# Kernel optimization log

Hardware: AMD Instinct MI355X
Metric: run time of the kernel (lower is better)

Reference implementation:

```python
import jax, jax.numpy as jnp
import numpy as np

B, S, D, DI = 8, 4096, 512, 2048
EPS = 1e-12  # torch F.normalize eps


def _l2norm(x):
    n = jnp.sqrt(jnp.sum(x * x, axis=-1, keepdims=True))
    return x / jnp.maximum(n, EPS)


def setup_inputs() -> dict:
    key = jax.random.key(0)
    ks = jax.random.split(key, 10)
    sd = 1.0 / np.sqrt(D)
    si = 1.0 / np.sqrt(DI)
    return {
        "x": jax.random.normal(ks[0], (B, S, D), jnp.float32),
        "wq": jax.random.uniform(ks[1], (D, DI), jnp.float32, -sd, sd),
        "wk": jax.random.uniform(ks[2], (D, DI), jnp.float32, -sd, sd),
        "wv": jax.random.uniform(ks[3], (D, DI), jnp.float32, -sd, sd),
        "wo": jax.random.uniform(ks[4], (DI, D), jnp.float32, -si, si),
        "w1": jax.random.uniform(ks[5], (D, DI), jnp.float32, -sd, sd),
        "b1": jax.random.uniform(ks[6], (DI,), jnp.float32, -sd, sd),
        "w2": jax.random.uniform(ks[7], (DI, D), jnp.float32, -si, si),
        "b2": jax.random.uniform(ks[8], (D,), jnp.float32, -si, si),
    }


def reference(x, wq, wk, wv, wo, w1, b1, w2, b2):
    # Hydra attention (linear): normalize(q) * sum_s(normalize(k)*v)
    q = _l2norm(jnp.einsum('bsd,de->bse', x, wq))
    k = _l2norm(jnp.einsum('bsd,de->bse', x, wk))
    v = jnp.einsum('bsd,de->bse', x, wv)
    kv = jnp.sum(k * v, axis=-2, keepdims=True)  # [B,1,DI]
    attn = jnp.einsum('bse,ed->bsd', q * kv, wo) + x  # dropout = identity (eval)
    # position-wise FFN with residual
    h = jax.nn.relu(jnp.einsum('bsd,de->bse', attn, w1) + b1)
    out = jnp.einsum('bse,ed->bsd', h, w2) + b2 + attn
    return out
```

## Files before the change

### kernel.cpp

```cpp
#include <hip/hip_runtime.h>
#include <stdint.h>

#define Bb  8
#define Ss  4096
#define Dd  512
#define DIi 2048
#define Mm  (Bb*Ss)

typedef unsigned short u16;
typedef __bf16 bf16x8 __attribute__((ext_vector_type(8)));
typedef float  f32x4  __attribute__((ext_vector_type(4)));

__device__ __forceinline__ float bfu(unsigned int u) {
  return __uint_as_float((u & 0xffffu) << 16);
}
__device__ __forceinline__ u16 f2bu(float f) {
  unsigned int x = __float_as_uint(f);
  return (u16)((x + 0x7fffu + ((x >> 16) & 1u)) >> 16);
}

__device__ __forceinline__ void tr_tile(const float* __restrict__ W, u16* __restrict__ Wt,
                                        int K, int N, int local, int tid) {
  __shared__ float t[32][33];
  const int nx = N / 32;
  const int n0 = (local % nx) * 32, k0 = (local / nx) * 32;
  const int tx = tid & 31, ty = tid >> 5;
#pragma unroll
  for (int i = 0; i < 32; i += 8)
    t[ty + i][tx] = W[(long)(k0 + ty + i) * N + n0 + tx];
  __syncthreads();
#pragma unroll
  for (int i = 0; i < 32; i += 8)
    Wt[(long)(n0 + ty + i) * K + k0 + tx] = f2bu(t[tx][ty + i]);
}

__global__ __launch_bounds__(256) void prep(
    const float* __restrict__ x, u16* __restrict__ xb,
    const float* wk, const float* wv, const float* w1,
    const float* wo, const float* w2, const float* wq,
    u16* wkT, u16* wvT, u16* w1T, u16* woT, u16* w2T, u16* wqb,
    float* __restrict__ zptr) {
  const int bid = blockIdx.x, tid = threadIdx.x;
  if (bid < 320) {
    zptr[bid * 256 + tid] = 0.f;
  } else if (bid < 2368) {
    long i = (long)(bid - 320) * 256 + tid;
    const long n4 = (long)Mm * Dd / 4;
    const long st = 2048L * 256;
    for (; i < n4; i += st) {
      float4 v = ((const float4*)x)[i];
      ushort4 o;
      o.x = f2bu(v.x); o.y = f2bu(v.y); o.z = f2bu(v.z); o.w = f2bu(v.w);
      ((ushort4*)xb)[i] = o;
    }
  } else if (bid < 3392)  tr_tile(wk, wkT, Dd, DIi, bid - 2368, tid);
  else if (bid < 4416)    tr_tile(wv, wvT, Dd, DIi, bid - 3392, tid);
  else if (bid < 5440)    tr_tile(w1, w1T, Dd, DIi, bid - 4416, tid);
  else if (bid < 6464)    tr_tile(wo, woT, DIi, Dd, bid - 5440, tid);
  else if (bid < 7488)    tr_tile(w2, w2T, DIi, Dd, bid - 6464, tid);
  else {
    long i = (long)(bid - 7488) * 256 + tid;
    float4 v = ((const float4*)wq)[i];
    ushort4 o;
    o.x = f2bu(v.x); o.y = f2bu(v.y); o.z = f2bu(v.z); o.w = f2bu(v.w);
    ((ushort4*)wqb)[i] = o;
  }
}

__global__ __launch_bounds__(256) void build_wob(const u16* __restrict__ woT,
                                                 const float* __restrict__ kv,
                                                 u16* __restrict__ wob) {
  const int b = blockIdx.y;
  long i = (long)blockIdx.x * 256 + threadIdx.x;
  const long tot = (long)Dd * DIi / 8;
  if (i >= tot) return;
  const long e = i * 8;
  const int k = (int)(e & (DIi - 1));
  ushort4 w0 = *(const ushort4*)(woT + e);
  ushort4 w1 = *(const ushort4*)(woT + e + 4);
  const float* kvp = kv + (long)b * DIi + k;
  ushort4 o0, o1;
  o0.x = f2bu(bfu(w0.x) * kvp[0]); o0.y = f2bu(bfu(w0.y) * kvp[1]);
  o0.z = f2bu(bfu(w0.z) * kvp[2]); o0.w = f2bu(bfu(w0.w) * kvp[3]);
  o1.x = f2bu(bfu(w1.x) * kvp[4]); o1.y = f2bu(bfu(w1.y) * kvp[5]);
  o1.z = f2bu(bfu(w1.z) * kvp[6]); o1.w = f2bu(bfu(w1.w) * kvp[7]);
  u16* dst = wob + (long)b * Dd * DIi + e;
  *(ushort4*)dst = o0;
  *(ushort4*)(dst + 4) = o1;
}

#define GLL(src, dst) \
  __builtin_amdgcn_global_load_lds((const __attribute__((address_space(1))) unsigned int*)(src), \
                                   (__attribute__((address_space(3))) unsigned int*)(dst), 16, 0, 0)

enum { G_PROJ = 0, G_FFN1 = 2, G_FFN2 = 3, G_KV = 4 };

template<int MODE>
__global__ __launch_bounds__(512, 2) void gemm8(
    const u16* __restrict__ A, const u16* __restrict__ Bt,
    int N, int K,
    u16* __restrict__ Ybf, float* __restrict__ Yf,
    const u16* __restrict__ resb, const float* __restrict__ bias,
    float* __restrict__ nsq, const float* __restrict__ nsqIn,
    const u16* __restrict__ Kst, float* __restrict__ kvout)
{
  __shared__ u16 lds8[65536];

  const int bx = blockIdx.x;
  const int by = blockIdx.y;
  const int tid  = threadIdx.x;
  const int lane = tid & 63;
  const int wid  = tid >> 6;
  const int wr = wid >> 2, wc = wid & 3;
  const int l15 = lane & 15, lg = lane >> 4;

  const long bm0 = (long)by * 256;
  const long bn0 = (long)bx * 256;
  const int NT = K >> 6;

  const int bq = (int)(bm0 >> 12);
  const u16* pA = A + bm0 * K;
  const u16* pB = Bt + bn0 * K;

  const int rowT = ((tid >> 6) << 3) | (tid & 7);
  const int cc8  = ((tid >> 3) & 7) * 8;

#define STAGE(PTR, LD, H, TT, BUFU, REGU) do {                                  \
    const u16* s0_ = (PTR) + (size_t)((H) * 128 + rowT) * (LD)                  \
                     + (size_t)(TT) * 64 + cc8;                                 \
    u16* d_ = lds8 + (BUFU) + (REGU) + (H) * 8192 + wid * 512;                  \
    GLL(s0_, d_);                                                               \
    GLL(s0_ + (size_t)64 * (LD), d_ + 4096);                                    \
  } while (0)

  const int aoff = (wr * 16384 + (l15 >> 3) * 1024 + lg * 128 + (l15 & 7) * 16) >> 1;
  const int boff = (32768 + (wc >> 1) * 16384 + (wc & 1) * 8192 +
                    (l15 >> 3) * 1024 + lg * 128 + (l15 & 7) * 16) >> 1;
#define LDA(M_, KS_, BU_) (*(const bf16x8*)(lds8 + (BU_) + aoff + (M_) * 1024 + (KS_) * 256))
#define LDB(N_, KS_, BU_) (*(const bf16x8*)(lds8 + (BU_) + boff + (N_) * 1024 + (KS_) * 256))

  f32x4 acc[8][4] = {};

  STAGE(pA, K, 0, 0, 0, 0);
  STAGE(pA, K, 1, 0, 0, 0);
  STAGE(pB, K, 0, 0, 0, 16384);
  STAGE(pB, K, 1, 0, 0, 16384);
  STAGE(pA, K, 0, 1, 32768, 0);
  asm volatile("s_waitcnt vmcnt(2)" ::: "memory");
  __builtin_amdgcn_s_barrier();

  for (int t = 0; t < NT; ++t) {
    const int bufu = (t & 1) * 32768;
    const int nbuf = bufu ^ 32768;
    bf16x8 aF[4], bF[4];

#pragma unroll
    for (int n = 0; n < 4; ++n) bF[n] = LDB(n, 0, bufu);
#pragma unroll
    for (int m = 0; m < 4; ++m) aF[m] = LDA(m, 0, bufu);
    if (t + 1 < NT) STAGE(pA, K, 1, t + 1, nbuf, 0);
    __builtin_amdgcn_s_barrier();
    __builtin_amdgcn_s_setprio(1);
#pragma unroll
    for (int m = 0; m < 4; ++m)
#pragma unroll
      for (int n = 0; n < 4; ++n)
        acc[m][n] = __builtin_amdgcn_mfma_f32_16x16x32_bf16(aF[m], bF[n], acc[m][n], 0, 0, 0);
    __builtin_amdgcn_s_setprio(0);

#pragma unroll
    for (int m = 0; m < 4; ++m) aF[m] = LDA(4 + m, 0, bufu);
    if (t + 1 < NT) STAGE(pB, K, 0, t + 1, nbuf, 16384);
    __builtin_amdgcn_s_barrier();
    __builtin_amdgcn_s_setprio(1);
#pragma unroll
    for (int m = 0; m < 4; ++m)
#pragma unroll
      for (int n = 0; n < 4; ++n)
        acc[4 + m][n] = __builtin_amdgcn_mfma_f32_16x16x32_bf16(aF[m], bF[n], acc[4 + m][n], 0, 0, 0);
    __builtin_amdgcn_s_setprio(0);

#pragma unroll
    for (int n = 0; n < 4; ++n) bF[n] = LDB(n, 1, bufu);
#pragma unroll
    for (int m = 0; m < 4; ++m) aF[m] = LDA(m, 1, bufu);
    if (t + 1 < NT) STAGE(pB, K, 1, t + 1, nbuf, 16384);
    __builtin_amdgcn_s_barrier();
    __builtin_amdgcn_s_setprio(1);
#pragma unroll
    for (int m = 0; m < 4; ++m)
#pragma unroll
      for (int n = 0; n < 4; ++n)
        acc[m][n] = __builtin_amdgcn_mfma_f32_16x16x32_bf16(aF[m], bF[n], acc[m][n], 0, 0, 0);
    __builtin_amdgcn_s_setprio(0);

#pragma unroll
    for (int m = 0; m < 4; ++m) aF[m] = LDA(4 + m, 1, bufu);
    __builtin_amdgcn_s_barrier();
    __builtin_amdgcn_s_setprio(1);
#pragma unroll
    for (int m = 0; m < 4; ++m)
#pragma unroll
      for (int n = 0; n < 4; ++n)
        acc[4 + m][n] = __builtin_amdgcn_mfma_f32_16x16x32_bf16(aF[m], bF[n], acc[4 + m][n], 0, 0, 0);
    __builtin_amdgcn_s_setprio(0);

    if (t + 1 < NT) {
      __builtin_amdgcn_s_barrier();
      if (t + 2 < NT) {
        STAGE(pA, K, 0, t + 2, bufu, 0);
        asm volatile("s_waitcnt vmcnt(2)" ::: "memory");
      } else {
        asm volatile("s_waitcnt vmcnt(0)" ::: "memory");
      }
      __builtin_amdgcn_s_barrier();
    }
  }

  if constexpr (MODE == G_KV) {
    __syncthreads();
#pragma unroll
    for (int i = 0; i < 16; ++i) {
      const int r_ = i * 16 + wid * 2 + (lane >> 5);
      const int c_ = (lane & 31) ^ (r_ & 15);
      const u16* src = Kst + (size_t)(bm0 + r_) * N + bn0 + c_ * 8;
      u16* d_ = lds8 + i * 4096 + wid * 512;
      GLL(src, d_);
    }
    asm volatile("s_waitcnt vmcnt(0)" ::: "memory");
    __builtin_amdgcn_s_barrier();

    const int col4 = wc * 64 + l15;
    float cs[4] = {0.f, 0.f, 0.f, 0.f};
#pragma unroll
    for (int m = 0; m < 8; ++m) {
      const long row0g = bm0 + wr * 128 + m * 16 + lg * 4;
      float rn4[4];
#pragma unroll
      for (int r = 0; r < 4; ++r)
        rn4[r] = 1.f / fmaxf(sqrtf(nsqIn[row0g + r]), 1e-12f);
#pragma unroll
      for (int n = 0; n < 4; ++n) {
        const int col = col4 + n * 16;
#pragma unroll
        for (int r = 0; r < 4; ++r) {
          const int krow = wr * 128 + m * 16 + lg * 4 + r;
          const int byte_ = krow * 512 + (((col >> 3) ^ (krow & 15)) << 4) + (col & 7) * 2;
          const float kvl = bfu(*(const u16*)((const char*)lds8 + byte_));
          cs[n] += kvl * rn4[r] * acc[m][n][r];
        }
      }
    }
#pragma unroll
    for (int n = 0; n < 4; ++n) {
      cs[n] += __shfl_xor(cs[n], 16, 64);
      cs[n] += __shfl_xor(cs[n], 32, 64);
    }
    if (lane < 16) {
#pragma unroll
      for (int n = 0; n < 4; ++n) {
        const long col = bn0 + wc * 64 + n * 16 + l15;
        atomicAdd(&kvout[(long)bq * DIi + col], cs[n]);
      }
    }
  } else if constexpr (MODE == G_PROJ) {
    float sk[32];
#pragma unroll
    for (int i = 0; i < 32; ++i) sk[i] = 0.f;
#pragma unroll
    for (int m = 0; m < 8; ++m) {
      const long row0 = bm0 + wr * 128 + m * 16 + lg * 4;
#pragma unroll
      for (int n = 0; n < 4; ++n) {
        const long col = bn0 + wc * 64 + n * 16 + l15;
#pragma unroll
        for (int r = 0; r < 4; ++r) {
          const float v = acc[m][n][r];
          Ybf[(row0 + r) * N + col] = f2bu(v);
          sk[m * 4 + r] += v * v;
        }
      }
    }
#pragma unroll
    for (int i = 0; i < 32; ++i) {
#pragma unroll
      for (int off = 1; off < 16; off <<= 1)
        sk[i] += __shfl_xor(sk[i], off, 64);
    }
    if (l15 == 0) {
#pragma unroll
      for (int m = 0; m < 8; ++m)
#pragma unroll
        for (int r = 0; r < 4; ++r)
          atomicAdd(&nsq[bm0 + wr * 128 + m * 16 + lg * 4 + r], sk[m * 4 + r]);
    }
  } else {
#pragma unroll
    for (int m = 0; m < 8; ++m) {
      const long row0 = bm0 + wr * 128 + m * 16 + lg * 4;
#pragma unroll
      for (int n = 0; n < 4; ++n) {
        const long col = bn0 + wc * 64 + n * 16 + l15;
#pragma unroll
        for (int r = 0; r < 4; ++r) {
          const long idx = (row0 + r) * N + col;
          const float v = acc[m][n][r];
          if constexpr (MODE == G_FFN1) {
            float o = v + bias[col];
            o = o > 0.f ? o : 0.f;
            Ybf[idx] = f2bu(o);
          } else {
            Yf[idx] = v + bias[col] + bfu(resb[idx]);
          }
        }
      }
    }
  }
#undef STAGE
#undef LDA
#undef LDB
}

__global__ __launch_bounds__(256) void mega_small(
    const u16* __restrict__ wqb, const u16* __restrict__ wob,
    u16* __restrict__ Gt, u16* __restrict__ Ut)
{
  __shared__ u16 As[4096];
  __shared__ u16 Bs[4096];
  const int K = DIi;
  const int z = blockIdx.z;
  const u16* Bt = (z == 0) ? wqb : wob + (size_t)(z - 1) * Dd * DIi;
  u16* Ct = (z == 0) ? Gt : Ut + (size_t)(z - 1) * Dd * Dd;

  const int tid = threadIdx.x, lane = tid & 63, w = tid >> 6;
  const int wr = w >> 1, wc = w & 1;
  const int l15 = lane & 15, lg = lane >> 4;
  const long bm0 = (long)blockIdx.y * 128;
  const long bn0 = (long)blockIdx.x * 128;

  const int c0 = tid, c1 = tid + 256;
  const u16* aS0 = wqb + (bm0 + (c0 >> 2)) * K + (c0 & 3) * 8;
  const u16* aS1 = wqb + (bm0 + (c1 >> 2)) * K + (c1 & 3) * 8;
  const u16* bS0 = Bt  + (bn0 + (c0 >> 2)) * K + (c0 & 3) * 8;
  const u16* bS1 = Bt  + (bn0 + (c1 >> 2)) * K + (c1 & 3) * 8;
  u16* aD0 = As + w * 512;
  u16* aD1 = As + 2048 + w * 512;
  u16* bD0 = Bs + w * 512;
  u16* bD1 = Bs + 2048 + w * 512;

  f32x4 acc[4][4] = {};

  for (int k0 = 0; k0 < K; k0 += 32) {
    GLL(aS0 + k0, aD0);
    GLL(aS1 + k0, aD1);
    GLL(bS0 + k0, bD0);
    GLL(bS1 + k0, bD1);
    __syncthreads();
    bf16x8 af[4], bfv[4];
#pragma unroll
    for (int m = 0; m < 4; ++m)
      af[m] = *(const bf16x8*)(As + (wr * 64 + m * 16 + l15) * 32 + lg * 8);
#pragma unroll
    for (int n = 0; n < 4; ++n)
      bfv[n] = *(const bf16x8*)(Bs + (wc * 64 + n * 16 + l15) * 32 + lg * 8);
#pragma unroll
    for (int m = 0; m < 4; ++m)
#pragma unroll
      for (int n = 0; n < 4; ++n)
        acc[m][n] = __builtin_amdgcn_mfma_f32_16x16x32_bf16(af[m], bfv[n], acc[m][n], 0, 0, 0);
    __syncthreads();
  }

#pragma unroll
  for (int m = 0; m < 4; ++m) {
    const int row0 = (int)bm0 + wr * 64 + m * 16 + lg * 4;
#pragma unroll
    for (int n = 0; n < 4; ++n) {
      const int col = (int)bn0 + wc * 64 + n * 16 + l15;
      ushort4 o;
      o.x = f2bu(acc[m][n][0]); o.y = f2bu(acc[m][n][1]);
      o.z = f2bu(acc[m][n][2]); o.w = f2bu(acc[m][n][3]);
      *(ushort4*)(Ct + (size_t)col * Dd + row0) = o;
    }
  }
}

template<int MODE>
__global__ __launch_bounds__(256) void mega_nx(
    const u16* __restrict__ xb, const u16* __restrict__ Gt, const u16* __restrict__ Ut,
    float* __restrict__ nqsq, u16* __restrict__ attnb)
{
  __shared__ u16 As[4096];
  __shared__ u16 Bs[4096];
  __shared__ u16 xs[16384];
  const int K = Dd, N = Dd;

  const int tid = threadIdx.x, lane = tid & 63, w = tid >> 6;
  const int wr = w >> 1, wc = w & 1;
  const int l15 = lane & 15, lg = lane >> 4;
  const long bm0 = (long)blockIdx.y * 128;
  const long bn0 = (long)blockIdx.x * 128;
  const int bq = (int)(bm0 >> 12);
  const u16* Bt = (MODE == 0) ? Gt : Ut + (size_t)bq * Dd * Dd;

  const int c0 = tid, c1 = tid + 256;
  const u16* aS0 = xb + (bm0 + (c0 >> 2)) * K + (c0 & 3) * 8;
  const u16* aS1 = xb + (bm0 + (c1 >> 2)) * K + (c1 & 3) * 8;
  const u16* bS0 = Bt + (bn0 + (c0 >> 2)) * K + (c0 & 3) * 8;
  const u16* bS1 = Bt + (bn0 + (c1 >> 2)) * K + (c1 & 3) * 8;
  u16* aD0 = As + w * 512;
  u16* aD1 = As + 2048 + w * 512;
  u16* bD0 = Bs + w * 512;
  u16* bD1 = Bs + 2048 + w * 512;

  f32x4 acc[4][4] = {};

  for (int k0 = 0; k0 < K; k0 += 32) {
    GLL(aS0 + k0, aD0);
    GLL(aS1 + k0, aD1);
    GLL(bS0 + k0, bD0);
    GLL(bS1 + k0, bD1);
    __syncthreads();
    bf16x8 af[4], bfv[4];
#pragma unroll
    for (int m = 0; m < 4; ++m)
      af[m] = *(const bf16x8*)(As + (wr * 64 + m * 16 + l15) * 32 + lg * 8);
#pragma unroll
    for (int n = 0; n < 4; ++n)
      bfv[n] = *(const bf16x8*)(Bs + (wc * 64 + n * 16 + l15) * 32 + lg * 8);
#pragma unroll
    for (int m = 0; m < 4; ++m)
#pragma unroll
      for (int n = 0; n < 4; ++n)
        acc[m][n] = __builtin_amdgcn_mfma_f32_16x16x32_bf16(af[m], bfv[n], acc[m][n], 0, 0, 0);
    __syncthreads();
  }

#pragma unroll
  for (int i = 0; i < 8; ++i) {
    const int c = i * 256 + tid;
    const int rowL = c >> 4;
    const int srcslot = (c & 15) ^ (rowL & 15);
    const u16* src = xb + (size_t)(bm0 + rowL) * Dd + bn0 + srcslot * 8;
    GLL(src, xs + i * 2048 + w * 512);
  }
  asm volatile("s_waitcnt vmcnt(0)" ::: "memory");
  __builtin_amdgcn_s_barrier();

#define XV(RL, CL) bfu(xs[(RL) * 128 + ((((CL) >> 3) ^ ((RL) & 15)) << 3) + ((CL) & 7)])

  if constexpr (MODE == 0) {
    float sk[16];
#pragma unroll
    for (int i = 0; i < 16; ++i) sk[i] = 0.f;
#pragma unroll
    for (int m = 0; m < 4; ++m) {
#pragma unroll
      for (int n = 0; n < 4; ++n) {
        const int colL = wc * 64 + n * 16 + l15;
#pragma unroll
        for (int r = 0; r < 4; ++r) {
          const int rowL = wr * 64 + m * 16 + lg * 4 + r;
          sk[m * 4 + r] += acc[m][n][r] * XV(rowL, colL);
        }
      }
    }
#pragma unroll
    for (int i = 0; i < 16; ++i) {
#pragma unroll
      for (int off = 1; off < 16; off <<= 1)
        sk[i] += __shfl_xor(sk[i], off, 64);
    }
    if (l15 == 0) {
#pragma unroll
      for (int m = 0; m < 4; ++m)
#pragma unroll
        for (int r = 0; r < 4; ++r)
          atomicAdd(&nqsq[bm0 + wr * 64 + m * 16 + lg * 4 + r], sk[m * 4 + r]);
    }
  } else {
#pragma unroll
    for (int m = 0; m < 4; ++m) {
      const long row0 = bm0 + wr * 64 + m * 16 + lg * 4;
      float rq[4];
#pragma unroll
      for (int r = 0; r < 4; ++r)
        rq[r] = 1.f / fmaxf(sqrtf(fmaxf(nqsq[row0 + r], 0.f)), 1e-12f);
#pragma unroll
      for (int n = 0; n < 4; ++n) {
        const int colL = wc * 64 + n * 16 + l15;
#pragma unroll
        for (int r = 0; r < 4; ++r) {
          const int rowL = wr * 64 + m * 16 + lg * 4 + r;
          attnb[(row0 + r) * N + bn0 + colL] = f2bu(acc[m][n][r] * rq[r] + XV(rowL, colL));
        }
      }
    }
  }
#undef XV
}

extern "C" void kernel_launch(void* const* d_in, const int* in_sizes, int n_in,
                              void* d_out, int out_size, void* d_ws, size_t ws_size,
                              hipStream_t stream) {
  const float* x  = (const float*)d_in[0];
  const float* wq = (const float*)d_in[1];
  const float* wk = (const float*)d_in[2];
  const float* wv = (const float*)d_in[3];
  const float* wo = (const float*)d_in[4];
  const float* w1 = (const float*)d_in[5];
  const float* b1 = (const float*)d_in[6];
  const float* w2 = (const float*)d_in[7];
  const float* b2 = (const float*)d_in[8];
  float* out = (float*)d_out;

  char* p = (char*)d_ws;
  auto take = [&](size_t bytes) {
    char* r = p; p += (bytes + 255) & ~(size_t)255; return r;
  };
  u16*   xb    = (u16*)take((size_t)Mm * Dd * 2);
  u16*   wkT   = (u16*)take((size_t)DIi * Dd * 2);
  u16*   wvT   = (u16*)take((size_t)DIi * Dd * 2);
  u16*   woT   = (u16*)take((size_t)Dd * DIi * 2);
  u16*   w1T   = (u16*)take((size_t)DIi * Dd * 2);
  u16*   w2T   = (u16*)take((size_t)Dd * DIi * 2);
  u16*   wqb   = (u16*)take((size_t)Dd * DIi * 2);
  u16*   wob   = (u16*)take((size_t)Bb * Dd * DIi * 2);
  u16*   Gt    = (u16*)take((size_t)Dd * Dd * 2);
  u16*   Ut    = (u16*)take((size_t)Bb * Dd * Dd * 2);
  u16*   buf1  = (u16*)take((size_t)Mm * DIi * 2);
  u16*   attnb = (u16*)take((size_t)Mm * Dd * 2);
  float* nksq  = (float*)take((size_t)Mm * 4);
  float* nqsq  = (float*)take((size_t)Mm * 4);
  float* kvp   = (float*)take((size_t)Bb * DIi * 4);
  (void)in_sizes; (void)n_in; (void)out_size; (void)ws_size;

  prep<<<8512, 256, 0, stream>>>(x, xb, wk, wv, w1, wo, w2, wq,
                                 wkT, wvT, w1T, woT, w2T, wqb, nksq);

  gemm8<G_PROJ><<<dim3(DIi / 256, Mm / 256), 512, 0, stream>>>(
      xb, wkT, DIi, Dd, buf1, nullptr, nullptr, nullptr, nksq, nullptr,
      nullptr, nullptr);

  gemm8<G_KV><<<dim3(DIi / 256, Mm / 256), 512, 0, stream>>>(
      xb, wvT, DIi, Dd, nullptr, nullptr, nullptr, nullptr, nullptr, nksq,
      buf1, kvp);

  build_wob<<<dim3((Dd * DIi / 8 + 255) / 256, Bb), 256, 0, stream>>>(woT, kvp, wob);

  mega_small<<<dim3(4, 4, 9), 256, 0, stream>>>(wqb, wob, Gt, Ut);

  mega_nx<0><<<dim3(4, Mm / 128), 256, 0, stream>>>(xb, Gt, nullptr, nqsq, nullptr);

  mega_nx<1><<<dim3(4, Mm / 128), 256, 0, stream>>>(xb, nullptr, Ut, nqsq, attnb);

  gemm8<G_FFN1><<<dim3(DIi / 256, Mm / 256), 512, 0, stream>>>(
      attnb, w1T, DIi, Dd, buf1, nullptr, nullptr, b1, nullptr, nullptr,
      nullptr, nullptr);

  gemm8<G_FFN2><<<dim3(Dd / 256, Mm / 256), 512, 0, stream>>>(
      buf1, w2T, Dd, DIi, nullptr, out, attnb, b2, nullptr, nullptr,
      nullptr, nullptr);
}
```

Before: 547.5 us.

## Compute key norms and kv via Gram matrices instead of full K/V projections

Removes the two full-size x·Wk and x·Wv GEMMs over all tokens. Key row norms now come from x·(Wk·Wkᵀ)·xᵀ through the existing Gram-style norm kernel. kv is computed as the column sums of Wk ∘ (Wvᵀ-side product of (x/|k|)ᵀ·x) per batch, using a transposed x, two small batched GEMMs and a column-sum kernel. This trades the large M×DI×D work for D×D×S per-batch GEMMs plus extra transposes and launches. Reassociating the sums in bf16 changes rounding.

```diff
diff --git a/kernel.cpp b/kernel.cpp
--- a/kernel.cpp
+++ b/kernel.cpp
@@ -36,15 +36,15 @@
 
 __global__ __launch_bounds__(256) void prep(
     const float* __restrict__ x, u16* __restrict__ xb,
-    const float* wk, const float* wv, const float* w1,
-    const float* wo, const float* w2, const float* wq,
-    u16* wkT, u16* wvT, u16* w1T, u16* woT, u16* w2T, u16* wqb,
+    const float* wv, const float* w1, const float* wo, const float* w2,
+    const float* wq, const float* wk,
+    u16* wvT, u16* w1T, u16* woT, u16* w2T, u16* wqb, u16* wkb,
     float* __restrict__ zptr) {
   const int bid = blockIdx.x, tid = threadIdx.x;
-  if (bid < 320) {
+  if (bid < 256) {
     zptr[bid * 256 + tid] = 0.f;
-  } else if (bid < 2368) {
-    long i = (long)(bid - 320) * 256 + tid;
+  } else if (bid < 2304) {
+    long i = (long)(bid - 256) * 256 + tid;
     const long n4 = (long)Mm * Dd / 4;
     const long st = 2048L * 256;
     for (; i < n4; i += st) {
@@ -53,17 +53,22 @@
       o.x = f2bu(v.x); o.y = f2bu(v.y); o.z = f2bu(v.z); o.w = f2bu(v.w);
       ((ushort4*)xb)[i] = o;
     }
-  } else if (bid < 3392)  tr_tile(wk, wkT, Dd, DIi, bid - 2368, tid);
-  else if (bid < 4416)    tr_tile(wv, wvT, Dd, DIi, bid - 3392, tid);
-  else if (bid < 5440)    tr_tile(w1, w1T, Dd, DIi, bid - 4416, tid);
-  else if (bid < 6464)    tr_tile(wo, woT, DIi, Dd, bid - 5440, tid);
-  else if (bid < 7488)    tr_tile(w2, w2T, DIi, Dd, bid - 6464, tid);
-  else {
-    long i = (long)(bid - 7488) * 256 + tid;
+  } else if (bid < 3328)  tr_tile(wv, wvT, Dd, DIi, bid - 2304, tid);
+  else if (bid < 4352)    tr_tile(w1, w1T, Dd, DIi, bid - 3328, tid);
+  else if (bid < 5376)    tr_tile(wo, woT, DIi, Dd, bid - 4352, tid);
+  else if (bid < 6400)    tr_tile(w2, w2T, DIi, Dd, bid - 5376, tid);
+  else if (bid < 7424) {
+    long i = (long)(bid - 6400) * 256 + tid;
     float4 v = ((const float4*)wq)[i];
     ushort4 o;
     o.x = f2bu(v.x); o.y = f2bu(v.y); o.z = f2bu(v.z); o.w = f2bu(v.w);
     ((ushort4*)wqb)[i] = o;
+  } else {
+    long i = (long)(bid - 7424) * 256 + tid;
+    float4 v = ((const float4*)wk)[i];
+    ushort4 o;
+    o.x = f2bu(v.x); o.y = f2bu(v.y); o.z = f2bu(v.z); o.w = f2bu(v.w);
+    ((ushort4*)wkb)[i] = o;
   }
 }
 
@@ -89,20 +94,65 @@
   *(ushort4*)(dst + 4) = o1;
 }
 
+__global__ void tr_x(const u16* __restrict__ xb, const float* __restrict__ nksq,
+                     u16* __restrict__ xT, u16* __restrict__ xrnT) {
+  __shared__ u16 t[32][33];
+  __shared__ float rns[32];
+  const int b = blockIdx.z;
+  const int s0 = blockIdx.y * 32, d0 = blockIdx.x * 32;
+  const int tx = threadIdx.x, ty = threadIdx.y;
+  const size_t sbase = (size_t)b * Ss + s0;
+#pragma unroll
+  for (int i = 0; i < 32; i += 8)
+    t[ty + i][tx] = xb[(sbase + ty + i) * Dd + d0 + tx];
+  if (ty == 0) {
+    const float nk = fmaxf(nksq[sbase + tx], 0.f);
+    rns[tx] = 1.f / fmaxf(sqrtf(nk), 1e-12f);
+  }
+  __syncthreads();
+  const size_t dbase = (size_t)b * Dd + d0;
+#pragma unroll
+  for (int i = 0; i < 32; i += 8) {
+    const u16 v = t[tx][ty + i];
+    const size_t idx = (dbase + ty + i) * Ss + s0 + tx;
+    xT[idx] = v;
+    xrnT[idx] = f2bu(bfu(v) * rns[tx]);
+  }
+}
+
+__global__ __launch_bounds__(256) void colsum_kv(const u16* __restrict__ wkb,
+                                                 const u16* __restrict__ Tb,
+                                                 float* __restrict__ kv) {
+  const int b = blockIdx.y;
+  const int e0 = blockIdx.x * 1024 + threadIdx.x * 4;
+  const u16* wp = wkb + e0;
+  const u16* tp = Tb + (size_t)b * Dd * DIi + e0;
+  float a0 = 0, a1 = 0, a2 = 0, a3 = 0;
+  for (int d = 0; d < Dd; ++d) {
+    ushort4 w = *(const ushort4*)wp;
+    ushort4 t = *(const ushort4*)tp;
+    a0 += bfu(w.x) * bfu(t.x);
+    a1 += bfu(w.y) * bfu(t.y);
+    a2 += bfu(w.z) * bfu(t.z);
+    a3 += bfu(w.w) * bfu(t.w);
+    wp += DIi; tp += DIi;
+  }
+  float* o = kv + (size_t)b * DIi + e0;
+  o[0] = a0; o[1] = a1; o[2] = a2; o[3] = a3;
+}
+
 #define GLL(src, dst) \
   __builtin_amdgcn_global_load_lds((const __attribute__((address_space(1))) unsigned int*)(src), \
                                    (__attribute__((address_space(3))) unsigned int*)(dst), 16, 0, 0)
 
-enum { G_PROJ = 0, G_FFN1 = 2, G_FFN2 = 3, G_KV = 4 };
+enum { G_FFN1 = 2, G_FFN2 = 3 };
 
 template<int MODE>
 __global__ __launch_bounds__(512, 2) void gemm8(
     const u16* __restrict__ A, const u16* __restrict__ Bt,
     int N, int K,
     u16* __restrict__ Ybf, float* __restrict__ Yf,
-    const u16* __restrict__ resb, const float* __restrict__ bias,
-    float* __restrict__ nsq, const float* __restrict__ nsqIn,
-    const u16* __restrict__ Kst, float* __restrict__ kvout)
+    const u16* __restrict__ resb, const float* __restrict__ bias)
 {
   __shared__ u16 lds8[65536];
 
@@ -118,7 +168,6 @@
   const long bn0 = (long)bx * 256;
   const int NT = K >> 6;
 
-  const int bq = (int)(bm0 >> 12);
   const u16* pA = A + bm0 * K;
   const u16* pB = Bt + bn0 * K;
 
@@ -217,101 +266,22 @@
     }
   }
 
-  if constexpr (MODE == G_KV) {
-    __syncthreads();
-#pragma unroll
-    for (int i = 0; i < 16; ++i) {
-      const int r_ = i * 16 + wid * 2 + (lane >> 5);
-      const int c_ = (lane & 31) ^ (r_ & 15);
-      const u16* src = Kst + (size_t)(bm0 + r_) * N + bn0 + c_ * 8;
-      u16* d_ = lds8 + i * 4096 + wid * 512;
-      GLL(src, d_);
-    }
-    asm volatile("s_waitcnt vmcnt(0)" ::: "memory");
-    __builtin_amdgcn_s_barrier();
-
-    const int col4 = wc * 64 + l15;
-    float cs[4] = {0.f, 0.f, 0.f, 0.f};
-#pragma unroll
-    for (int m = 0; m < 8; ++m) {
-      const long row0g = bm0 + wr * 128 + m * 16 + lg * 4;
-      float rn4[4];
-#pragma unroll
-      for (int r = 0; r < 4; ++r)
-        rn4[r] = 1.f / fmaxf(sqrtf(nsqIn[row0g + r]), 1e-12f);
-#pragma unroll
-      for (int n = 0; n < 4; ++n) {
-        const int col = col4 + n * 16;
-#pragma unroll
-        for (int r = 0; r < 4; ++r) {
-          const int krow = wr * 128 + m * 16 + lg * 4 + r;
-          const int byte_ = krow * 512 + (((col >> 3) ^ (krow & 15)) << 4) + (col & 7) * 2;
-          const float kvl = bfu(*(const u16*)((const char*)lds8 + byte_));
-          cs[n] += kvl * rn4[r] * acc[m][n][r];
-        }
-      }
-    }
+#pragma unroll
+  for (int m = 0; m < 8; ++m) {
+    const long row0 = bm0 + wr * 128 + m * 16 + lg * 4;
 #pragma unroll
     for (int n = 0; n < 4; ++n) {
-      cs[n] += __shfl_xor(cs[n], 16, 64);
-      cs[n] += __shfl_xor(cs[n], 32, 64);
-    }
-    if (lane < 16) {
-#pragma unroll
-      for (int n = 0; n < 4; ++n) {
-        const long col = bn0 + wc * 64 + n * 16 + l15;
-        atomicAdd(&kvout[(long)bq * DIi + col], cs[n]);
-      }
-    }
-  } else if constexpr (MODE == G_PROJ) {
-    float sk[32];
-#pragma unroll
-    for (int i = 0; i < 32; ++i) sk[i] = 0.f;
-#pragma unroll
-    for (int m = 0; m < 8; ++m) {
-      const long row0 = bm0 + wr * 128 + m * 16 + lg * 4;
-#pragma unroll
-      for (int n = 0; n < 4; ++n) {
-        const long col = bn0 + wc * 64 + n * 16 + l15;
-#pragma unroll
-        for (int r = 0; r < 4; ++r) {
-          const float v = acc[m][n][r];
-          Ybf[(row0 + r) * N + col] = f2bu(v);
-          sk[m * 4 + r] += v * v;
-        }
-      }
-    }
-#pragma unroll
-    for (int i = 0; i < 32; ++i) {
-#pragma unroll
-      for (int off = 1; off < 16; off <<= 1)
-        sk[i] += __shfl_xor(sk[i], off, 64);
-    }
-    if (l15 == 0) {
-#pragma unroll
-      for (int m = 0; m < 8; ++m)
-#pragma unroll
-        for (int r = 0; r < 4; ++r)
-          atomicAdd(&nsq[bm0 + wr * 128 + m * 16 + lg * 4 + r], sk[m * 4 + r]);
-    }
-  } else {
-#pragma unroll
-    for (int m = 0; m < 8; ++m) {
-      const long row0 = bm0 + wr * 128 + m * 16 + lg * 4;
-#pragma unroll
-      for (int n = 0; n < 4; ++n) {
-        const long col = bn0 + wc * 64 + n * 16 + l15;
-#pragma unroll
-        for (int r = 0; r < 4; ++r) {
-          const long idx = (row0 + r) * N + col;
-          const float v = acc[m][n][r];
-          if constexpr (MODE == G_FFN1) {
-            float o = v + bias[col];
-            o = o > 0.f ? o : 0.f;
-            Ybf[idx] = f2bu(o);
-          } else {
-            Yf[idx] = v + bias[col] + bfu(resb[idx]);
-          }
+      const long col = bn0 + wc * 64 + n * 16 + l15;
+#pragma unroll
+      for (int r = 0; r < 4; ++r) {
+        const long idx = (row0 + r) * N + col;
+        const float v = acc[m][n][r];
+        if constexpr (MODE == G_FFN1) {
+          float o = v + bias[col];
+          o = o > 0.f ? o : 0.f;
+          Ybf[idx] = f2bu(o);
+        } else {
+          Yf[idx] = v + bias[col] + bfu(resb[idx]);
         }
       }
     }
@@ -322,15 +292,19 @@
 }
 
 __global__ __launch_bounds__(256) void mega_small(
-    const u16* __restrict__ wqb, const u16* __restrict__ wob,
-    u16* __restrict__ Gt, u16* __restrict__ Ut)
+    const u16* __restrict__ wqb, const u16* __restrict__ wkb,
+    const u16* __restrict__ wob,
+    u16* __restrict__ Gt, u16* __restrict__ Gkt, u16* __restrict__ Ut, int zbase)
 {
   __shared__ u16 As[4096];
   __shared__ u16 Bs[4096];
   const int K = DIi;
-  const int z = blockIdx.z;
-  const u16* Bt = (z == 0) ? wqb : wob + (size_t)(z - 1) * Dd * DIi;
-  u16* Ct = (z == 0) ? Gt : Ut + (size_t)(z - 1) * Dd * Dd;
+  const int idx = blockIdx.z + zbase;
+  const u16* A  = (idx == 1) ? wkb : wqb;
+  const u16* Bt = (idx == 0) ? wqb : (idx == 1) ? wkb
+                  : wob + (size_t)(idx - 2) * Dd * DIi;
+  u16* Ct = (idx == 0) ? Gt : (idx == 1) ? Gkt
+            : Ut + (size_t)(idx - 2) * Dd * Dd;
 
   const int tid = threadIdx.x, lane = tid & 63, w = tid >> 6;
   const int wr = w >> 1, wc = w & 1;
@@ -339,10 +313,10 @@
   const long bn0 = (long)blockIdx.x * 128;
 
   const int c0 = tid, c1 = tid + 256;
-  const u16* aS0 = wqb + (bm0 + (c0 >> 2)) * K + (c0 & 3) * 8;
-  const u16* aS1 = wqb + (bm0 + (c1 >> 2)) * K + (c1 & 3) * 8;
-  const u16* bS0 = Bt  + (bn0 + (c0 >> 2)) * K + (c0 & 3) * 8;
-  const u16* bS1 = Bt  + (bn0 + (c1 >> 2)) * K + (c1 & 3) * 8;
+  const u16* aS0 = A  + (bm0 + (c0 >> 2)) * K + (c0 & 3) * 8;
+  const u16* aS1 = A  + (bm0 + (c1 >> 2)) * K + (c1 & 3) * 8;
+  const u16* bS0 = Bt + (bn0 + (c0 >> 2)) * K + (c0 & 3) * 8;
+  const u16* bS1 = Bt + (bn0 + (c1 >> 2)) * K + (c1 & 3) * 8;
   u16* aD0 = As + w * 512;
   u16* aD1 = As + 2048 + w * 512;
   u16* bD0 = Bs + w * 512;
@@ -386,9 +360,74 @@
 }
 
 template<int MODE>
+__global__ __launch_bounds__(256) void mega128b(
+    const u16* __restrict__ A0, const u16* __restrict__ Bt0,
+    u16* __restrict__ C0, int N, int K)
+{
+  __shared__ u16 As[4096];
+  __shared__ u16 Bs[4096];
+  const int z = blockIdx.z;
+  const u16* A  = A0 + (size_t)z * (MODE == 0 ? (size_t)Dd * Ss : (size_t)Dd * Dd);
+  const u16* Bt = (MODE == 0) ? Bt0 + (size_t)z * Dd * Ss : Bt0;
+  u16* C = C0 + (size_t)z * (MODE == 0 ? (size_t)Dd * Dd : (size_t)Dd * DIi);
+
+  const int tid = threadIdx.x, lane = tid & 63, w = tid >> 6;
+  const int wr = w >> 1, wc = w & 1;
+  const int l15 = lane & 15, lg = lane >> 4;
+  const long bm0 = (long)blockIdx.y * 128;
+  const long bn0 = (long)blockIdx.x * 128;
+
+  const int c0 = tid, c1 = tid + 256;
+  const u16* aS0 = A  + (bm0 + (c0 >> 2)) * K + (c0 & 3) * 8;
+  const u16* aS1 = A  + (bm0 + (c1 >> 2)) * K + (c1 & 3) * 8;
+  const u16* bS0 = Bt + (bn0 + (c0 >> 2)) * K + (c0 & 3) * 8;
+  const u16* bS1 = Bt + (bn0 + (c1 >> 2)) * K + (c1 & 3) * 8;
+  u16* aD0 = As + w * 512;
+  u16* aD1 = As + 2048 + w * 512;
+  u16* bD0 = Bs + w * 512;
+  u16* bD1 = Bs + 2048 + w * 512;
+
+  f32x4 acc[4][4] = {};
+
+  for (int k0 = 0; k0 < K; k0 += 32) {
+    GLL(aS0 + k0, aD0);
+    GLL(aS1 + k0, aD1);
+    GLL(bS0 + k0, bD0);
+    GLL(bS1 + k0, bD1);
+    __syncthreads();
+    bf16x8 af[4], bfv[4];
+#pragma unroll
+    for (int m = 0; m < 4; ++m)
+      af[m] = *(const bf16x8*)(As + (wr * 64 + m * 16 + l15) * 32 + lg * 8);
+#pragma unroll
+    for (int n = 0; n < 4; ++n)
+      bfv[n] = *(const bf16x8*)(Bs + (wc * 64 + n * 16 + l15) * 32 + lg * 8);
+#pragma unroll
+    for (int m = 0; m < 4; ++m)
+#pragma unroll
+      for (int n = 0; n < 4; ++n)
+        acc[m][n] = __builtin_amdgcn_mfma_f32_16x16x32_bf16(af[m], bfv[n], acc[m][n], 0, 0, 0);
+    __syncthreads();
+  }
+
+#pragma unroll
+  for (int m = 0; m < 4; ++m) {
+    const long row0 = bm0 + wr * 64 + m * 16 + lg * 4;
+#pragma unroll
+    for (int n = 0; n < 4; ++n) {
+      const long col = bn0 + wc * 64 + n * 16 + l15;
+#pragma unroll
+      for (int r = 0; r < 4; ++r)
+        C[(row0 + r) * N + col] = f2bu(acc[m][n][r]);
+    }
+  }
+}
+
+template<int MODE>
 __global__ __launch_bounds__(256) void mega_nx(
-    const u16* __restrict__ xb, const u16* __restrict__ Gt, const u16* __restrict__ Ut,
-    float* __restrict__ nqsq, u16* __restrict__ attnb)
+    const u16* __restrict__ xb, const u16* __restrict__ Gt, const u16* __restrict__ Gkt,
+    const u16* __restrict__ Ut,
+    float* __restrict__ nqsq, float* __restrict__ nksq, u16* __restrict__ attnb)
 {
   __shared__ u16 As[4096];
   __shared__ u16 Bs[4096];
@@ -398,10 +437,12 @@
   const int tid = threadIdx.x, lane = tid & 63, w = tid >> 6;
   const int wr = w >> 1, wc = w & 1;
   const int l15 = lane & 15, lg = lane >> 4;
-  const long bm0 = (long)blockIdx.y * 128;
+  const bool isK = (MODE == 0) && (blockIdx.y >= Mm / 128);
+  const long bm0 = (long)(isK ? blockIdx.y - Mm / 128 : blockIdx.y) * 128;
   const long bn0 = (long)blockIdx.x * 128;
   const int bq = (int)(bm0 >> 12);
-  const u16* Bt = (MODE == 0) ? Gt : Ut + (size_t)bq * Dd * Dd;
+  const u16* Bt = (MODE == 0) ? (isK ? Gkt : Gt) : Ut + (size_t)bq * Dd * Dd;
+  float* nsq = (MODE == 0) ? (isK ? nksq : nqsq) : nqsq;
 
   const int c0 = tid, c1 = tid + 256;
   const u16* aS0 = xb + (bm0 + (c0 >> 2)) * K + (c0 & 3) * 8;
@@ -476,7 +517,7 @@
       for (int m = 0; m < 4; ++m)
 #pragma unroll
         for (int r = 0; r < 4; ++r)
-          atomicAdd(&nqsq[bm0 + wr * 64 + m * 16 + lg * 4 + r], sk[m * 4 + r]);
+          atomicAdd(&nsq[bm0 + wr * 64 + m * 16 + lg * 4 + r], sk[m * 4 + r]);
     }
   } else {
 #pragma unroll
@@ -519,46 +560,54 @@
     char* r = p; p += (bytes + 255) & ~(size_t)255; return r;
   };
   u16*   xb    = (u16*)take((size_t)Mm * Dd * 2);
-  u16*   wkT   = (u16*)take((size_t)DIi * Dd * 2);
   u16*   wvT   = (u16*)take((size_t)DIi * Dd * 2);
+  u16*   w1T   = (u16*)take((size_t)DIi * Dd * 2);
   u16*   woT   = (u16*)take((size_t)Dd * DIi * 2);
-  u16*   w1T   = (u16*)take((size_t)DIi * Dd * 2);
   u16*   w2T   = (u16*)take((size_t)Dd * DIi * 2);
   u16*   wqb   = (u16*)take((size_t)Dd * DIi * 2);
-  u16*   wob   = (u16*)take((size_t)Bb * Dd * DIi * 2);
+  u16*   wkb   = (u16*)take((size_t)Dd * DIi * 2);
   u16*   Gt    = (u16*)take((size_t)Dd * Dd * 2);
+  u16*   Gkt   = (u16*)take((size_t)Dd * Dd * 2);
   u16*   Ut    = (u16*)take((size_t)Bb * Dd * Dd * 2);
   u16*   buf1  = (u16*)take((size_t)Mm * DIi * 2);
   u16*   attnb = (u16*)take((size_t)Mm * Dd * 2);
   float* nksq  = (float*)take((size_t)Mm * 4);
   float* nqsq  = (float*)take((size_t)Mm * 4);
   float* kvp   = (float*)take((size_t)Bb * DIi * 4);
+  u16* xT   = buf1;
+  u16* xrnT = buf1 + (size_t)Mm * Dd;
+  u16* Tb   = buf1 + 2 * (size_t)Mm * Dd;
+  u16* Cb   = buf1 + 2 * (size_t)Mm * Dd + (size_t)Bb * Dd * DIi;
+  u16* wob  = buf1 + 2 * (size_t)Mm * Dd + (size_t)Bb * Dd * DIi
+                   + (size_t)Bb * Dd * Dd;
   (void)in_sizes; (void)n_in; (void)out_size; (void)ws_size;
 
-  prep<<<8512, 256, 0, stream>>>(x, xb, wk, wv, w1, wo, w2, wq,
-                                 wkT, wvT, w1T, woT, w2T, wqb, nksq);
-
-  gemm8<G_PROJ><<<dim3(DIi / 256, Mm / 256), 512, 0, stream>>>(
-      xb, wkT, DIi, Dd, buf1, nullptr, nullptr, nullptr, nksq, nullptr,
-      nullptr, nullptr);
-
-  gemm8<G_KV><<<dim3(DIi / 256, Mm / 256), 512, 0, stream>>>(
-      xb, wvT, DIi, Dd, nullptr, nullptr, nullptr, nullptr, nullptr, nksq,
-      buf1, kvp);
-
-  build_wob<<<dim3((Dd * DIi / 8 + 255) / 256, Bb), 256, 0, stream>>>(woT, kvp, wob);
-
-  mega_small<<<dim3(4, 4, 9), 256, 0, stream>>>(wqb, wob, Gt, Ut);
-
-  mega_nx<0><<<dim3(4, Mm / 128), 256, 0, stream>>>(xb, Gt, nullptr, nqsq, nullptr);
-
-  mega_nx<1><<<dim3(4, Mm / 128), 256, 0, stream>>>(xb, nullptr, Ut, nqsq, attnb);
+  prep<<<8448, 256, 0, stream>>>(x, xb, wv, w1, wo, w2, wq, wk,
+                                 wvT, w1T, woT, w2T, wqb, wkb, nksq);
+
+  mega_small<<<dim3(4, 4, 2), 256, 0, stream>>>(wqb, wkb, nullptr, Gt, Gkt, Ut, 0);
+
+  mega_nx<0><<<dim3(4, 2 * Mm / 128), 256, 0, stream>>>(
+      xb, Gt, Gkt, nullptr, nqsq, nksq, nullptr);
+
+  tr_x<<<dim3(Dd / 32, Ss / 32, Bb), dim3(32, 8), 0, stream>>>(xb, nksq, xT, xrnT);
+
+  mega128b<0><<<dim3(4, 4, Bb), 256, 0, stream>>>(xrnT, xT, Cb, Dd, Ss);
+
+  mega128b<1><<<dim3(16, 4, Bb), 256, 0, stream>>>(Cb, wvT, Tb, DIi, Dd);
+
+  colsum_kv<<<dim3(2, Bb), 256, 0, stream>>>(wkb, Tb, kvp);
+
+  build_wob<<<dim3(512, Bb), 256, 0, stream>>>(woT, kvp, wob);
+
+  mega_small<<<dim3(4, 4, 8), 256, 0, stream>>>(wqb, wkb, wob, Gt, Gkt, Ut, 2);
+
+  mega_nx<1><<<dim3(4, Mm / 128), 256, 0, stream>>>(
+      xb, nullptr, nullptr, Ut, nqsq, nullptr, attnb);
 
   gemm8<G_FFN1><<<dim3(DIi / 256, Mm / 256), 512, 0, stream>>>(
-      attnb, w1T, DIi, Dd, buf1, nullptr, nullptr, b1, nullptr, nullptr,
-      nullptr, nullptr);
+      attnb, w1T, DIi, Dd, buf1, nullptr, nullptr, b1);
 
   gemm8<G_FFN2><<<dim3(Dd / 256, Mm / 256), 512, 0, stream>>>(
-      buf1, w2T, Dd, DIi, nullptr, out, attnb, b2, nullptr, nullptr,
-      nullptr, nullptr);
-}
+      buf1, w2T, Dd, DIi, nullptr, out, attnb, b2);
+}
```

New measurement: 552.7 us. Within noise of the previous version (+1.0%).
